# Kernel optimization log

Measured on AMD Instinct MI355X. Metric: run time of the kernel, lower is better.

The kernel has to match this reference:

```python
import jax, jax.numpy as jnp
import numpy as np
import math

# Static configuration (matches init_kwargs / input_specs)
L1 = 2          # lmax of x
L2 = 2          # lmax of y
LZ = L1 + L2    # output lmax = 4
RB = 20         # res_beta (Gauss-Legendre nodes)
RA = 19         # res_alpha (uniform azimuthal samples)
MUL = 128       # input multiplicity per l
C = 128         # num_channels
N = 1024        # batch (nodes/edges)


def _assoc_legendre(l, m, x):
    """Associated Legendre P_l^m(x) with Condon-Shortley phase, via recurrence."""
    pmm = np.ones_like(x)
    if m > 0:
        dfact = float(np.prod(np.arange(1, 2 * m, 2)))  # (2m-1)!!
        pmm = ((-1.0) ** m) * dfact * (1.0 - x * x) ** (m / 2.0)
    if l == m:
        return pmm
    pmmp1 = x * (2 * m + 1) * pmm
    if l == m + 1:
        return pmmp1
    for ll in range(m + 2, l + 1):
        p = ((2 * ll - 1) * x * pmmp1 - (ll + m - 1) * pmm) / (ll - m)
        pmm, pmmp1 = pmmp1, p
    return pmmp1


def _sh_table(L, rb, ra):
    """Orthonormal real spherical harmonics sampled on the (beta, alpha) grid.

    Returns Y [(L+1)^2, rb, ra] and Gauss-Legendre weights qw [rb] such that
    sum_{b,a} f(b,a) Y_lm(b,a) qw[b] * (2*pi/ra) == c_lm exactly for
    bandlimited f (the inverse of the synthesis c -> grid).
    """
    ct, qw = np.polynomial.legendre.leggauss(rb)  # nodes = cos(beta)
    alpha = 2.0 * np.pi * np.arange(ra) / ra
    Y = np.zeros(((L + 1) ** 2, rb, ra))
    for l in range(L + 1):
        for m in range(-l, l + 1):
            am = abs(m)
            nlm = math.sqrt((2 * l + 1) / (4 * math.pi)
                            * math.factorial(l - am) / math.factorial(l + am))
            P = _assoc_legendre(l, am, ct)  # [rb]
            if m == 0:
                ang = np.ones(ra)
            elif m > 0:
                ang = math.sqrt(2.0) * np.cos(m * alpha)
            else:
                ang = math.sqrt(2.0) * np.sin(am * alpha)
            Y[l * l + l + m] = nlm * P[:, None] * ang[None, :]
    return Y, qw


_Y_np, _QW_np = _sh_table(LZ, RB, RA)
Y_TAB = jnp.asarray(_Y_np, jnp.float32)   # [(LZ+1)^2, RB, RA]
QW = jnp.asarray(_QW_np, jnp.float32)     # [RB]


def _per_l_linear_in(v, w, L):
    """Equivariant per-l linear: v [N, mul, (L+1)^2], w [L+1, mul, C] -> [N, C, (L+1)^2]."""
    scale = 1.0 / math.sqrt(v.shape[1])
    outs = [jnp.einsum('nmd,mc->ncd', v[..., l * l:(l + 1) ** 2], w[l]) * scale
            for l in range(L + 1)]
    return jnp.concatenate(outs, axis=-1)


def setup_inputs() -> dict:
    key = jax.random.key(0)
    k0, k1, k2, k3, k4 = jax.random.split(key, 5)
    return {
        'x': jax.random.normal(k0, (N, MUL, (L1 + 1) ** 2), jnp.float32),
        'y': jax.random.normal(k1, (N, MUL, (L2 + 1) ** 2), jnp.float32),
        'wx': jax.random.normal(k2, (L1 + 1, MUL, C), jnp.float32),
        'wy': jax.random.normal(k3, (L2 + 1, MUL, C), jnp.float32),
        'wz': jax.random.normal(k4, (LZ + 1, C, C), jnp.float32),
    }


def reference(x, y, wx, wy, wz):
    # linear_in + mul_to_axis: [N, mul, D] -> [N, C, D]
    xc = _per_l_linear_in(x, wx, L1)  # [N, C, 9]
    yc = _per_l_linear_in(y, wy, L2)  # [N, C, 9]

    # to_s2grid (synthesis): coeffs -> signal on (beta, alpha) grid
    gx = jnp.einsum('ncd,dba->ncba', xc, Y_TAB[:(L1 + 1) ** 2])  # [N,C,RB,RA]
    gy = jnp.einsum('ncd,dba->ncba', yc, Y_TAB[:(L2 + 1) ** 2])

    # pointwise Gaunt product on the grid
    prod = gx * gy

    # from_s2grid (analysis): quadrature projection onto Y_lm up to LZ
    z = jnp.einsum('ncba,dba,b->ncd', prod, Y_TAB, QW) * (2.0 * jnp.pi / RA)  # [N,C,25]

    # axis_to_mul + linear_out_z: per-l channel mixing [C -> C]
    scale = 1.0 / math.sqrt(C)
    outs = [jnp.einsum('ncd,ce->ned', z[..., l * l:(l + 1) ** 2], wz[l]) * scale
            for l in range(LZ + 1)]
    return jnp.concatenate(outs, axis=-1)  # [N, C, 25]
```

## Files before the change

kernel.cpp:

```cpp
#include <hip/hip_runtime.h>
#include <cmath>

#define RB 20
#define RA 19
#define NPT (RB*RA)
#define DZ 25
#define DIN 9
#define MULT 128
#define CH 128

__host__ __device__ constexpr int L_of(int d) { return d == 0 ? 0 : d < 4 ? 1 : d < 9 ? 2 : d < 16 ? 3 : 4; }
__host__ __device__ constexpr int M_of(int d) { return d - L_of(d) * L_of(d) - L_of(d); }
__host__ __device__ constexpr bool gz_nz(int d1, int d2, int dz) {
    const int l1 = L_of(d1), l2 = L_of(d2), l3 = L_of(dz);
    const int m1 = M_of(d1), m2 = M_of(d2), m3 = M_of(dz);
    const int lo = l1 > l2 ? l1 - l2 : l2 - l1;
    if (l3 < lo || l3 > l1 + l2) return false;
    if ((l1 + l2 + l3) & 1) return false;
    const int a1 = m1 < 0 ? -m1 : m1, a2 = m2 < 0 ? -m2 : m2, a3 = m3 < 0 ? -m3 : m3;
    const int sum = a1 + a2, dif = a1 > a2 ? a1 - a2 : a2 - a1;
    if (a3 != sum && a3 != dif) return false;
    if (((m1 < 0) + (m2 < 0) + (m3 < 0)) & 1) return false;
    return true;
}
template<int DZ0, int DZ1>
__host__ __device__ constexpr bool pair_any_r(int d1, int d2) {
    for (int dz = DZ0; dz < DZ1; ++dz) if (gz_nz(d1, d2, dz)) return true;
    return false;
}

static void host_build_gaunt(float* out ) {
    const double PI = 3.14159265358979323846;
    double xq[RB], wq[RB];
    for (int i = 0; i < RB; ++i) {
        double x = cos(PI * (i + 0.75) / (RB + 0.5));
        double dp = 0.0;
        for (int it = 0; it < 100; ++it) {
            double p0 = 1.0, p1 = x;
            for (int k = 2; k <= RB; ++k) {
                double p2 = ((2.0*k - 1.0)*x*p1 - (k - 1.0)*p0) / (double)k;
                p0 = p1; p1 = p2;
            }
            dp = RB * (x*p1 - p0) / (x*x - 1.0);
            double dx = p1 / dp;
            x -= dx;
            if (fabs(dx) < 1e-15) break;
        }
        {
            double p0 = 1.0, p1 = x;
            for (int k = 2; k <= RB; ++k) {
                double p2 = ((2.0*k - 1.0)*x*p1 - (k - 1.0)*p0) / (double)k;
                p0 = p1; p1 = p2;
            }
            dp = RB * (x*p1 - p0) / (x*x - 1.0);
        }
        xq[i] = x;
        wq[i] = 2.0 / ((1.0 - x*x)*dp*dp);
    }
    static double Y[DZ][NPT];
    static double qws[NPT];
    for (int b = 0; b < RB; ++b) {
        double ct = xq[b], st = sqrt(fmax(0.0, 1.0 - ct*ct));
        double P[5][5]; double pmm = 1.0;
        for (int m = 0; m <= 4; ++m) {
            if (m > 0) pmm *= -(2.0*m - 1.0) * st;
            P[m][m] = pmm;
            if (m < 4) {
                double pp = pmm, pc = ct*(2.0*m + 1.0)*pmm;
                P[m+1][m] = pc;
                for (int l = m + 2; l <= 4; ++l) {
                    double pn = ((2.0*l - 1.0)*ct*pc - (double)(l + m - 1)*pp) / (double)(l - m);
                    P[l][m] = pn; pp = pc; pc = pn;
                }
            }
        }
        for (int a = 0; a < RA; ++a) {
            int pt = b*RA + a;
            qws[pt] = wq[b] * (2.0*PI/(double)RA);
            double alpha = 2.0*PI*(double)a/(double)RA;
            for (int l = 0; l <= 4; ++l)
                for (int m = -l; m <= l; ++m) {
                    int am = m < 0 ? -m : m;
                    double fr = 1.0;
                    for (int i = l - am + 1; i <= l + am; ++i) fr *= (double)i;
                    double nlm = sqrt((2.0*l + 1.0) / (4.0*PI) / fr);
                    double ang = (m == 0) ? 1.0
                               : (m > 0 ? sqrt(2.0)*cos(am*alpha) : sqrt(2.0)*sin(am*alpha));
                    Y[l*l + l + m][pt] = nlm * P[l][am] * ang;
                }
        }
    }
    for (int pr = 0; pr < 81; ++pr) {
        int d1 = pr / 9, d2 = pr % 9;
        for (int d = 0; d < DZ; ++d) {
            double s = 0.0;
            for (int p = 0; p < NPT; ++p)
                s += Y[d][p] * Y[d1][p] * Y[d2][p] * qws[p];
            out[pr*28 + d] = gz_nz(d1, d2, d) ? (float)s : 0.0f;
        }
    }
}

template<int DZ0, int DZ1, int D1, int D2, int DZi>
__device__ __forceinline__ void c_dz(const float* __restrict__ g, float p0, float p1,
                                     float* a0, float* a1) {
    if constexpr (DZi < DZ1) {
        if constexpr (gz_nz(D1, D2, DZi)) {
            const float gv = g[(D1 * 9 + D2) * 28 + DZi];
            a0[DZi - DZ0] = fmaf(p0, gv, a0[DZi - DZ0]);
            a1[DZi - DZ0] = fmaf(p1, gv, a1[DZi - DZ0]);
        }
        c_dz<DZ0, DZ1, D1, D2, DZi + 1>(g, p0, p1, a0, a1);
    }
}
template<int DZ0, int DZ1, int D1, int D2>
__device__ __forceinline__ void c_d2(const float* __restrict__ g,
                                     const float* x0, const float* x1,
                                     const float* y0, const float* y1,
                                     float* a0, float* a1) {
    if constexpr (D2 < 9) {
        if constexpr (pair_any_r<DZ0, DZ1>(D1, D2))
            c_dz<DZ0, DZ1, D1, D2, DZ0>(g, x0[D1] * y0[D2], x1[D1] * y1[D2], a0, a1);
        c_d2<DZ0, DZ1, D1, D2 + 1>(g, x0, x1, y0, y1, a0, a1);
    }
}
template<int DZ0, int DZ1, int D1>
__device__ __forceinline__ void c_d1(const float* __restrict__ g,
                                     const float* x0, const float* x1,
                                     const float* y0, const float* y1,
                                     float* a0, float* a1) {
    if constexpr (D1 < 9) {
        c_d2<DZ0, DZ1, D1, 0>(g, x0, x1, y0, y1, a0, a1);
        c_d1<DZ0, DZ1, D1 + 1>(g, x0, x1, y0, y1, a0, a1);
    }
}

template<int D0, int ND, int L0, int NL>
__device__ __forceinline__ void d_tile(const float* sZ, const float* __restrict__ wz,
                                       float* __restrict__ po, int lane) {
    const float s128 = 0.08838834764831845f;
    const int e2 = lane << 1;
    float acc[ND * 4];
    #pragma unroll
    for (int i = 0; i < ND * 4; ++i) acc[i] = 0.f;
    float2 wA[NL * 4], wB[NL * 4];

    #define LOADW_D(W, C0) { \
        _Pragma("unroll") \
        for (int j = 0; j < NL; ++j) { \
            _Pragma("unroll") \
            for (int k = 0; k < 4; ++k) \
                W[j * 4 + k] = *(const float2*)(wz + (L0 + j) * 16384 + ((C0) + k) * 128 + e2); \
        } }
    #define FMA_D(W, C0) { \
        _Pragma("unroll") \
        for (int i = 0; i < ND; ++i) { \
            const int d = D0 + i; \
            const int l = (d == 0) ? 0 : (d < 4) ? 1 : (d < 9) ? 2 : (d < 16) ? 3 : 4; \
            float4 z0 = *(const float4*)(sZ + d * 128 + (C0));           \
            float4 z1 = *(const float4*)(sZ + (25 + d) * 128 + (C0));    \
            _Pragma("unroll") \
            for (int k = 0; k < 4; ++k) { \
                float zc0 = (k == 0) ? z0.x : (k == 1) ? z0.y : (k == 2) ? z0.z : z0.w; \
                float zc1 = (k == 0) ? z1.x : (k == 1) ? z1.y : (k == 2) ? z1.z : z1.w; \
                acc[i*4+0] = fmaf(zc0, W[(l - L0) * 4 + k].x, acc[i*4+0]); \
                acc[i*4+1] = fmaf(zc0, W[(l - L0) * 4 + k].y, acc[i*4+1]); \
                acc[i*4+2] = fmaf(zc1, W[(l - L0) * 4 + k].x, acc[i*4+2]); \
                acc[i*4+3] = fmaf(zc1, W[(l - L0) * 4 + k].y, acc[i*4+3]); \
            } \
        } }

    LOADW_D(wA, 0);
    for (int c0 = 0; c0 < CH; c0 += 8) {
        LOADW_D(wB, c0 + 4);
        FMA_D(wA, c0);
        if (c0 < CH - 8) LOADW_D(wA, c0 + 8);
        FMA_D(wB, c0 + 4);
    }
    #undef LOADW_D
    #undef FMA_D

    #pragma unroll
    for (int i = 0; i < ND; ++i) {
        po[e2 * 25 + D0 + i]              = acc[i*4+0] * s128;
        po[(e2 + 1) * 25 + D0 + i]        = acc[i*4+1] * s128;
        po[3200 + e2 * 25 + D0 + i]       = acc[i*4+2] * s128;
        po[3200 + (e2 + 1) * 25 + D0 + i] = acc[i*4+3] * s128;
    }
}

__global__ __launch_bounds__(256) void gaunt_fused(
    const float* __restrict__ xg, const float* __restrict__ yg,
    const float* __restrict__ wxg, const float* __restrict__ wyg,
    const float* __restrict__ wzg, float* __restrict__ outg,
    const float* __restrict__ gGt) {

    __shared__ __align__(16) float pool[17884];
    float* sZ  = pool;
    float* sXY = pool + 6400;
    float* sXc = pool + 11008;
    float* sG  = pool + 15616;

    const int tid  = threadIdx.x;
    const int b    = blockIdx.x;
    const int lane = tid & 63;
    const int wave = __builtin_amdgcn_readfirstlane(tid >> 6);
    const float s128 = 0.08838834764831845f;

    {
        const float4* xs = (const float4*)(xg + 2 * b * 1152);
        const float4* ys = (const float4*)(yg + 2 * b * 1152);
        for (int i = tid; i < 1152; i += 256) {
            float4 v = (i < 576) ? xs[i] : ys[i - 576];
            int r = (i < 576) ? i : i - 576;
            int base = (i < 576) ? 0 : 2304;
            int j0 = r * 4;
            #pragma unroll
            for (int k = 0; k < 4; ++k) {
                int j = j0 + k;
                int n = j / 1152;
                int jj = j - n * 1152;
                int m = jj / 9, d = jj - 9 * m;
                float val = (k == 0) ? v.x : (k == 1) ? v.y : (k == 2) ? v.z : v.w;
                sXY[base + n * 1152 + d * 128 + m] = val;
            }
        }
        for (int i = tid; i < 567; i += 256)
            ((float4*)sG)[i] = ((const float4*)gGt)[i];
    }
    __syncthreads();

    {
        const int side = wave >> 1, n = wave & 1;
        const int c2 = lane << 1;
        const float* wb = side ? wyg : wxg;
        const float* xb = sXY + side * 2304 + n * 1152;
        float acc[18];
        #pragma unroll
        for (int i = 0; i < 18; ++i) acc[i] = 0.f;
        float2 wA[12], wB[12];

        #define LOADW_B(W, M0) { \
            _Pragma("unroll") \
            for (int k = 0; k < 4; ++k) { \
                W[k]     = *(const float2*)(wb + ((M0) + k) * 128 + c2); \
                W[4 + k] = *(const float2*)(wb + 16384 + ((M0) + k) * 128 + c2); \
                W[8 + k] = *(const float2*)(wb + 32768 + ((M0) + k) * 128 + c2); \
            } }
        #define FMA_B(W, M0) { \
            _Pragma("unroll") \
            for (int d = 0; d < 9; ++d) { \
                const int lb = (d == 0) ? 0 : (d < 4) ? 4 : 8; \
                float4 xv = *(const float4*)(xb + d * 128 + (M0));    \
                acc[d*2+0] = fmaf(xv.x, W[lb+0].x, acc[d*2+0]); \
                acc[d*2+0] = fmaf(xv.y, W[lb+1].x, acc[d*2+0]); \
                acc[d*2+0] = fmaf(xv.z, W[lb+2].x, acc[d*2+0]); \
                acc[d*2+0] = fmaf(xv.w, W[lb+3].x, acc[d*2+0]); \
                acc[d*2+1] = fmaf(xv.x, W[lb+0].y, acc[d*2+1]); \
                acc[d*2+1] = fmaf(xv.y, W[lb+1].y, acc[d*2+1]); \
                acc[d*2+1] = fmaf(xv.z, W[lb+2].y, acc[d*2+1]); \
                acc[d*2+1] = fmaf(xv.w, W[lb+3].y, acc[d*2+1]); \
            } }

        LOADW_B(wA, 0);
        for (int m0 = 0; m0 < MULT; m0 += 8) {
            LOADW_B(wB, m0 + 4);
            FMA_B(wA, m0);
            if (m0 < MULT - 8) LOADW_B(wA, m0 + 8);
            FMA_B(wB, m0 + 4);
        }
        #undef LOADW_B
        #undef FMA_B

        #pragma unroll
        for (int d = 0; d < 9; ++d) {
            float2 v = make_float2(acc[d*2+0] * s128, acc[d*2+1] * s128);
            *(float2*)(sXc + ((side * 9 + d) * 2 + n) * 128 + c2) = v;
        }
    }
    __syncthreads();

    {
        const int c = tid & 127;
        const int half = __builtin_amdgcn_readfirstlane(tid >> 7);
        float xr0[9], xr1[9], yr0[9], yr1[9];
        #pragma unroll
        for (int d = 0; d < 9; ++d) {
            xr0[d] = sXc[(d * 2 + 0) * 128 + c];
            xr1[d] = sXc[(d * 2 + 1) * 128 + c];
            yr0[d] = sXc[((9 + d) * 2 + 0) * 128 + c];
            yr1[d] = sXc[((9 + d) * 2 + 1) * 128 + c];
        }
        if (half == 0) {
            float a0[12], a1[12];
            #pragma unroll
            for (int i = 0; i < 12; ++i) { a0[i] = 0.f; a1[i] = 0.f; }
            c_d1<0, 12, 0>(sG, xr0, xr1, yr0, yr1, a0, a1);
            #pragma unroll
            for (int i = 0; i < 12; ++i) {
                sZ[i * 128 + c]        = a0[i];
                sZ[(25 + i) * 128 + c] = a1[i];
            }
        } else {
            float a0[13], a1[13];
            #pragma unroll
            for (int i = 0; i < 13; ++i) { a0[i] = 0.f; a1[i] = 0.f; }
            c_d1<12, 25, 0>(sG, xr0, xr1, yr0, yr1, a0, a1);
            #pragma unroll
            for (int i = 0; i < 13; ++i) {
                sZ[(12 + i) * 128 + c] = a0[i];
                sZ[(37 + i) * 128 + c] = a1[i];
            }
        }
    }
    __syncthreads();

    float* po = outg + 2 * b * (CH * DZ);
    if      (wave == 0) d_tile<0,  4, 0, 2>(sZ, wzg, po, lane);
    else if (wave == 1) d_tile<4,  5, 2, 1>(sZ, wzg, po, lane);
    else if (wave == 2) d_tile<9,  7, 3, 1>(sZ, wzg, po, lane);
    else                d_tile<16, 9, 4, 1>(sZ, wzg, po, lane);
}

extern "C" void kernel_launch(void* const* d_in, const int* in_sizes, int n_in,
                              void* d_out, int out_size, void* d_ws, size_t ws_size,
                              hipStream_t stream) {
    static float h_gGt[81 * 28];
    static bool built = false;
    if (!built) { host_build_gaunt(h_gGt); built = true; }
    hipMemcpyAsync(d_ws, h_gGt, sizeof(h_gGt), hipMemcpyHostToDevice, stream);

    int N = in_sizes[0] / (MULT * DIN);

    hipLaunchKernelGGL(gaunt_fused, dim3(N / 2), dim3(256), 0, stream,
                       (const float*)d_in[0], (const float*)d_in[1],
                       (const float*)d_in[2], (const float*)d_in[3],
                       (const float*)d_in[4], (float*)d_out, (const float*)d_ws);
}
```

Baseline: 115.4 us.

## Process four nodes per block to amortize weight loads across more rows

Each block now handles four batch rows instead of two. Every weight element loaded from global memory in the input-linear and output-linear stages is reused across four nodes, which halves weight traffic per node. The cost is larger shared memory (about 134KB), more accumulators per thread, and a launch bound of one block per CU. The grid also shrinks to 256 blocks, which lowers occupancy and latency hiding on a GPU with many CUs.

```diff
diff --git a/kernel.cpp b/kernel.cpp
--- a/kernel.cpp
+++ b/kernel.cpp
@@ -136,13 +136,13 @@
 }
 
 template<int D0, int ND, int L0, int NL>
-__device__ __forceinline__ void d_tile(const float* sZ, const float* __restrict__ wz,
-                                       float* __restrict__ po, int lane) {
+__device__ __forceinline__ void d_tile4(const float* sZ, const float* __restrict__ wz,
+                                        float* __restrict__ outp, int lane) {
     const float s128 = 0.08838834764831845f;
     const int e2 = lane << 1;
-    float acc[ND * 4];
+    float acc[ND * 8];
     #pragma unroll
-    for (int i = 0; i < ND * 4; ++i) acc[i] = 0.f;
+    for (int i = 0; i < ND * 8; ++i) acc[i] = 0.f;
     float2 wA[NL * 4], wB[NL * 4];
 
     #define LOADW_D(W, C0) { \
@@ -157,63 +157,63 @@
         for (int i = 0; i < ND; ++i) { \
             const int d = D0 + i; \
             const int l = (d == 0) ? 0 : (d < 4) ? 1 : (d < 9) ? 2 : (d < 16) ? 3 : 4; \
-            float4 z0 = *(const float4*)(sZ + d * 128 + (C0));           \
-            float4 z1 = *(const float4*)(sZ + (25 + d) * 128 + (C0));    \
             _Pragma("unroll") \
-            for (int k = 0; k < 4; ++k) { \
-                float zc0 = (k == 0) ? z0.x : (k == 1) ? z0.y : (k == 2) ? z0.z : z0.w; \
-                float zc1 = (k == 0) ? z1.x : (k == 1) ? z1.y : (k == 2) ? z1.z : z1.w; \
-                acc[i*4+0] = fmaf(zc0, W[(l - L0) * 4 + k].x, acc[i*4+0]); \
-                acc[i*4+1] = fmaf(zc0, W[(l - L0) * 4 + k].y, acc[i*4+1]); \
-                acc[i*4+2] = fmaf(zc1, W[(l - L0) * 4 + k].x, acc[i*4+2]); \
-                acc[i*4+3] = fmaf(zc1, W[(l - L0) * 4 + k].y, acc[i*4+3]); \
+            for (int n = 0; n < 4; ++n) { \
+                float4 z4 = *(const float4*)(sZ + (n * 25 + d) * 128 + (C0));   \
+                _Pragma("unroll") \
+                for (int k = 0; k < 4; ++k) { \
+                    float zc = (k == 0) ? z4.x : (k == 1) ? z4.y : (k == 2) ? z4.z : z4.w; \
+                    acc[(i*4+n)*2+0] = fmaf(zc, W[(l - L0) * 4 + k].x, acc[(i*4+n)*2+0]); \
+                    acc[(i*4+n)*2+1] = fmaf(zc, W[(l - L0) * 4 + k].y, acc[(i*4+n)*2+1]); \
+                } \
             } \
         } }
 
     LOADW_D(wA, 0);
+    LOADW_D(wB, 4);
     for (int c0 = 0; c0 < CH; c0 += 8) {
-        LOADW_D(wB, c0 + 4);
         FMA_D(wA, c0);
-        if (c0 < CH - 8) LOADW_D(wA, c0 + 8);
+        if (c0 + 8 < CH) LOADW_D(wA, c0 + 8);
         FMA_D(wB, c0 + 4);
+        if (c0 + 12 < CH) LOADW_D(wB, c0 + 12);
     }
     #undef LOADW_D
     #undef FMA_D
 
     #pragma unroll
-    for (int i = 0; i < ND; ++i) {
-        po[e2 * 25 + D0 + i]              = acc[i*4+0] * s128;
-        po[(e2 + 1) * 25 + D0 + i]        = acc[i*4+1] * s128;
-        po[3200 + e2 * 25 + D0 + i]       = acc[i*4+2] * s128;
-        po[3200 + (e2 + 1) * 25 + D0 + i] = acc[i*4+3] * s128;
-    }
-}
-
-__global__ __launch_bounds__(256) void gaunt_fused(
+    for (int i = 0; i < ND; ++i)
+        #pragma unroll
+        for (int n = 0; n < 4; ++n) {
+            outp[n * 3200 + e2 * 25 + D0 + i]       = acc[(i*4+n)*2+0] * s128;
+            outp[n * 3200 + (e2 + 1) * 25 + D0 + i] = acc[(i*4+n)*2+1] * s128;
+        }
+}
+
+__global__ __launch_bounds__(256, 1) void gaunt_fused(
     const float* __restrict__ xg, const float* __restrict__ yg,
     const float* __restrict__ wxg, const float* __restrict__ wyg,
     const float* __restrict__ wzg, float* __restrict__ outg,
     const float* __restrict__ gGt) {
 
-    __shared__ __align__(16) float pool[17884];
-    float* sZ  = pool;
-    float* sXY = pool + 6400;
-    float* sXc = pool + 11008;
-    float* sG  = pool + 15616;
+    __shared__ __align__(16) float pool[33500];
+    float* sXY = pool;
+    float* sXc = pool + 9216;
+    float* sZ  = pool + 18432;
+    float* sG  = pool + 31232;
 
     const int tid  = threadIdx.x;
-    const int b    = blockIdx.x;
+    const int nb4  = blockIdx.x * 4;
     const int lane = tid & 63;
     const int wave = __builtin_amdgcn_readfirstlane(tid >> 6);
     const float s128 = 0.08838834764831845f;
 
     {
-        const float4* xs = (const float4*)(xg + 2 * b * 1152);
-        const float4* ys = (const float4*)(yg + 2 * b * 1152);
-        for (int i = tid; i < 1152; i += 256) {
-            float4 v = (i < 576) ? xs[i] : ys[i - 576];
-            int r = (i < 576) ? i : i - 576;
-            int base = (i < 576) ? 0 : 2304;
+        const float4* xs = (const float4*)(xg + (size_t)nb4 * 1152);
+        const float4* ys = (const float4*)(yg + (size_t)nb4 * 1152);
+        for (int i = tid; i < 2304; i += 256) {
+            float4 v = (i < 1152) ? xs[i] : ys[i - 1152];
+            int r = (i < 1152) ? i : i - 1152;
+            int base = (i < 1152) ? 0 : 4608;
             int j0 = r * 4;
             #pragma unroll
             for (int k = 0; k < 4; ++k) {
@@ -231,95 +231,98 @@
     __syncthreads();
 
     {
-        const int side = wave >> 1, n = wave & 1;
-        const int c2 = lane << 1;
+        const int side = wave >> 1, ch = wave & 1;
+        const int c = ch * 64 + lane;
         const float* wb = side ? wyg : wxg;
-        const float* xb = sXY + side * 2304 + n * 1152;
-        float acc[18];
+        const float* xb = sXY + side * 4608;
+        float acc[36];
         #pragma unroll
-        for (int i = 0; i < 18; ++i) acc[i] = 0.f;
-        float2 wA[12], wB[12];
+        for (int i = 0; i < 36; ++i) acc[i] = 0.f;
+        float wA[12], wB[12];
 
         #define LOADW_B(W, M0) { \
             _Pragma("unroll") \
             for (int k = 0; k < 4; ++k) { \
-                W[k]     = *(const float2*)(wb + ((M0) + k) * 128 + c2); \
-                W[4 + k] = *(const float2*)(wb + 16384 + ((M0) + k) * 128 + c2); \
-                W[8 + k] = *(const float2*)(wb + 32768 + ((M0) + k) * 128 + c2); \
+                W[k]     = wb[((M0) + k) * 128 + c]; \
+                W[4 + k] = wb[16384 + ((M0) + k) * 128 + c]; \
+                W[8 + k] = wb[32768 + ((M0) + k) * 128 + c]; \
             } }
         #define FMA_B(W, M0) { \
             _Pragma("unroll") \
             for (int d = 0; d < 9; ++d) { \
                 const int lb = (d == 0) ? 0 : (d < 4) ? 4 : 8; \
-                float4 xv = *(const float4*)(xb + d * 128 + (M0));    \
-                acc[d*2+0] = fmaf(xv.x, W[lb+0].x, acc[d*2+0]); \
-                acc[d*2+0] = fmaf(xv.y, W[lb+1].x, acc[d*2+0]); \
-                acc[d*2+0] = fmaf(xv.z, W[lb+2].x, acc[d*2+0]); \
-                acc[d*2+0] = fmaf(xv.w, W[lb+3].x, acc[d*2+0]); \
-                acc[d*2+1] = fmaf(xv.x, W[lb+0].y, acc[d*2+1]); \
-                acc[d*2+1] = fmaf(xv.y, W[lb+1].y, acc[d*2+1]); \
-                acc[d*2+1] = fmaf(xv.z, W[lb+2].y, acc[d*2+1]); \
-                acc[d*2+1] = fmaf(xv.w, W[lb+3].y, acc[d*2+1]); \
+                _Pragma("unroll") \
+                for (int n = 0; n < 4; ++n) { \
+                    float4 xv = *(const float4*)(xb + n * 1152 + d * 128 + (M0));   \
+                    acc[d*4+n] = fmaf(xv.x, W[lb+0], acc[d*4+n]); \
+                    acc[d*4+n] = fmaf(xv.y, W[lb+1], acc[d*4+n]); \
+                    acc[d*4+n] = fmaf(xv.z, W[lb+2], acc[d*4+n]); \
+                    acc[d*4+n] = fmaf(xv.w, W[lb+3], acc[d*4+n]); \
+                } \
             } }
 
         LOADW_B(wA, 0);
+        LOADW_B(wB, 4);
         for (int m0 = 0; m0 < MULT; m0 += 8) {
-            LOADW_B(wB, m0 + 4);
             FMA_B(wA, m0);
-            if (m0 < MULT - 8) LOADW_B(wA, m0 + 8);
+            if (m0 + 8 < MULT) LOADW_B(wA, m0 + 8);
             FMA_B(wB, m0 + 4);
+            if (m0 + 12 < MULT) LOADW_B(wB, m0 + 12);
         }
         #undef LOADW_B
         #undef FMA_B
 
         #pragma unroll
-        for (int d = 0; d < 9; ++d) {
-            float2 v = make_float2(acc[d*2+0] * s128, acc[d*2+1] * s128);
-            *(float2*)(sXc + ((side * 9 + d) * 2 + n) * 128 + c2) = v;
-        }
+        for (int d = 0; d < 9; ++d)
+            #pragma unroll
+            for (int n = 0; n < 4; ++n)
+                sXc[((side * 9 + d) * 4 + n) * 128 + c] = acc[d*4+n] * s128;
     }
     __syncthreads();
 
     {
         const int c = tid & 127;
         const int half = __builtin_amdgcn_readfirstlane(tid >> 7);
-        float xr0[9], xr1[9], yr0[9], yr1[9];
         #pragma unroll
-        for (int d = 0; d < 9; ++d) {
-            xr0[d] = sXc[(d * 2 + 0) * 128 + c];
-            xr1[d] = sXc[(d * 2 + 1) * 128 + c];
-            yr0[d] = sXc[((9 + d) * 2 + 0) * 128 + c];
-            yr1[d] = sXc[((9 + d) * 2 + 1) * 128 + c];
-        }
-        if (half == 0) {
-            float a0[12], a1[12];
+        for (int np = 0; np < 2; ++np) {
+            float xr0[9], xr1[9], yr0[9], yr1[9];
             #pragma unroll
-            for (int i = 0; i < 12; ++i) { a0[i] = 0.f; a1[i] = 0.f; }
-            c_d1<0, 12, 0>(sG, xr0, xr1, yr0, yr1, a0, a1);
-            #pragma unroll
-            for (int i = 0; i < 12; ++i) {
-                sZ[i * 128 + c]        = a0[i];
-                sZ[(25 + i) * 128 + c] = a1[i];
-            }
-        } else {
-            float a0[13], a1[13];
-            #pragma unroll
-            for (int i = 0; i < 13; ++i) { a0[i] = 0.f; a1[i] = 0.f; }
-            c_d1<12, 25, 0>(sG, xr0, xr1, yr0, yr1, a0, a1);
-            #pragma unroll
-            for (int i = 0; i < 13; ++i) {
-                sZ[(12 + i) * 128 + c] = a0[i];
-                sZ[(37 + i) * 128 + c] = a1[i];
+            for (int d = 0; d < 9; ++d) {
+                xr0[d] = sXc[(d * 4 + np * 2 + 0) * 128 + c];
+                xr1[d] = sXc[(d * 4 + np * 2 + 1) * 128 + c];
+                yr0[d] = sXc[((9 + d) * 4 + np * 2 + 0) * 128 + c];
+                yr1[d] = sXc[((9 + d) * 4 + np * 2 + 1) * 128 + c];
+            }
+            if (half == 0) {
+                float a0[12], a1[12];
+                #pragma unroll
+                for (int i = 0; i < 12; ++i) { a0[i] = 0.f; a1[i] = 0.f; }
+                c_d1<0, 12, 0>(sG, xr0, xr1, yr0, yr1, a0, a1);
+                #pragma unroll
+                for (int i = 0; i < 12; ++i) {
+                    sZ[((np * 2 + 0) * 25 + i) * 128 + c] = a0[i];
+                    sZ[((np * 2 + 1) * 25 + i) * 128 + c] = a1[i];
+                }
+            } else {
+                float a0[13], a1[13];
+                #pragma unroll
+                for (int i = 0; i < 13; ++i) { a0[i] = 0.f; a1[i] = 0.f; }
+                c_d1<12, 25, 0>(sG, xr0, xr1, yr0, yr1, a0, a1);
+                #pragma unroll
+                for (int i = 0; i < 13; ++i) {
+                    sZ[((np * 2 + 0) * 25 + 12 + i) * 128 + c] = a0[i];
+                    sZ[((np * 2 + 1) * 25 + 12 + i) * 128 + c] = a1[i];
+                }
             }
         }
     }
     __syncthreads();
 
-    float* po = outg + 2 * b * (CH * DZ);
-    if      (wave == 0) d_tile<0,  4, 0, 2>(sZ, wzg, po, lane);
-    else if (wave == 1) d_tile<4,  5, 2, 1>(sZ, wzg, po, lane);
-    else if (wave == 2) d_tile<9,  7, 3, 1>(sZ, wzg, po, lane);
-    else                d_tile<16, 9, 4, 1>(sZ, wzg, po, lane);
+    float* po = outg + (size_t)nb4 * (CH * DZ);
+    if      (wave == 0) d_tile4<0,  4, 0, 2>(sZ, wzg, po, lane);
+    else if (wave == 1) d_tile4<4,  5, 2, 1>(sZ, wzg, po, lane);
+    else if (wave == 2) d_tile4<9,  7, 3, 1>(sZ, wzg, po, lane);
+    else                d_tile4<16, 9, 4, 1>(sZ, wzg, po, lane);
 }
 
 extern "C" void kernel_launch(void* const* d_in, const int* in_sizes, int n_in,
@@ -332,7 +335,7 @@
 
     int N = in_sizes[0] / (MULT * DIN);
 
-    hipLaunchKernelGGL(gaunt_fused, dim3(N / 2), dim3(256), 0, stream,
+    hipLaunchKernelGGL(gaunt_fused, dim3(N / 4), dim3(256), 0, stream,
                        (const float*)d_in[0], (const float*)d_in[1],
                        (const float*)d_in[2], (const float*)d_in[3],
                        (const float*)d_in[4], (float*)d_out, (const float*)d_ws);
```

After: 122.8 us. 1.06x slower.

## Drop LDS transpose, remap linear-in to channel-per-lane, deepen weight prefetch

Applied to the files above, without the earlier changes.

The input staging now copies x and y into shared memory in their native [n][m][d] order instead of transposing into d-major layout. The linear-in stage is remapped so each lane owns one channel for both nodes, reading the inputs via broadcast float4 LDS loads. Weight loads in both matmul stages change from float2 per lane to two scalar loads, with four register buffers for a deeper prefetch. Launch bounds now request 2 blocks per SM, which may force register spilling given the larger register arrays.

```diff
diff --git a/kernel.cpp b/kernel.cpp
--- a/kernel.cpp
+++ b/kernel.cpp
@@ -139,18 +139,19 @@
 __device__ __forceinline__ void d_tile(const float* sZ, const float* __restrict__ wz,
                                        float* __restrict__ po, int lane) {
     const float s128 = 0.08838834764831845f;
-    const int e2 = lane << 1;
     float acc[ND * 4];
     #pragma unroll
     for (int i = 0; i < ND * 4; ++i) acc[i] = 0.f;
-    float2 wA[NL * 4], wB[NL * 4];
+    float W0[NL * 8], W1[NL * 8], W2[NL * 8], W3[NL * 8];
 
     #define LOADW_D(W, C0) { \
         _Pragma("unroll") \
         for (int j = 0; j < NL; ++j) { \
             _Pragma("unroll") \
-            for (int k = 0; k < 4; ++k) \
-                W[j * 4 + k] = *(const float2*)(wz + (L0 + j) * 16384 + ((C0) + k) * 128 + e2); \
+            for (int k = 0; k < 4; ++k) { \
+                W[j*8 + k*2 + 0] = wz[(L0 + j) * 16384 + ((C0) + k) * 128 + lane]; \
+                W[j*8 + k*2 + 1] = wz[(L0 + j) * 16384 + ((C0) + k) * 128 + lane + 64]; \
+            } \
         } }
     #define FMA_D(W, C0) { \
         _Pragma("unroll") \
@@ -161,35 +162,37 @@
             float4 z1 = *(const float4*)(sZ + (25 + d) * 128 + (C0));    \
             _Pragma("unroll") \
             for (int k = 0; k < 4; ++k) { \
+                float wa = W[(l - L0)*8 + k*2 + 0]; \
+                float wb = W[(l - L0)*8 + k*2 + 1]; \
                 float zc0 = (k == 0) ? z0.x : (k == 1) ? z0.y : (k == 2) ? z0.z : z0.w; \
                 float zc1 = (k == 0) ? z1.x : (k == 1) ? z1.y : (k == 2) ? z1.z : z1.w; \
-                acc[i*4+0] = fmaf(zc0, W[(l - L0) * 4 + k].x, acc[i*4+0]); \
-                acc[i*4+1] = fmaf(zc0, W[(l - L0) * 4 + k].y, acc[i*4+1]); \
-                acc[i*4+2] = fmaf(zc1, W[(l - L0) * 4 + k].x, acc[i*4+2]); \
-                acc[i*4+3] = fmaf(zc1, W[(l - L0) * 4 + k].y, acc[i*4+3]); \
+                acc[i*4+0] = fmaf(zc0, wa, acc[i*4+0]); \
+                acc[i*4+1] = fmaf(zc0, wb, acc[i*4+1]); \
+                acc[i*4+2] = fmaf(zc1, wa, acc[i*4+2]); \
+                acc[i*4+3] = fmaf(zc1, wb, acc[i*4+3]); \
             } \
         } }
 
-    LOADW_D(wA, 0);
-    for (int c0 = 0; c0 < CH; c0 += 8) {
-        LOADW_D(wB, c0 + 4);
-        FMA_D(wA, c0);
-        if (c0 < CH - 8) LOADW_D(wA, c0 + 8);
-        FMA_D(wB, c0 + 4);
+    LOADW_D(W0, 0); LOADW_D(W1, 4); LOADW_D(W2, 8); LOADW_D(W3, 12);
+    for (int c0 = 0; c0 < CH; c0 += 16) {
+        FMA_D(W0, c0);        if (c0 + 16 < CH) LOADW_D(W0, c0 + 16);
+        FMA_D(W1, c0 + 4);    if (c0 + 20 < CH) LOADW_D(W1, c0 + 20);
+        FMA_D(W2, c0 + 8);    if (c0 + 24 < CH) LOADW_D(W2, c0 + 24);
+        FMA_D(W3, c0 + 12);   if (c0 + 28 < CH) LOADW_D(W3, c0 + 28);
     }
     #undef LOADW_D
     #undef FMA_D
 
     #pragma unroll
     for (int i = 0; i < ND; ++i) {
-        po[e2 * 25 + D0 + i]              = acc[i*4+0] * s128;
-        po[(e2 + 1) * 25 + D0 + i]        = acc[i*4+1] * s128;
-        po[3200 + e2 * 25 + D0 + i]       = acc[i*4+2] * s128;
-        po[3200 + (e2 + 1) * 25 + D0 + i] = acc[i*4+3] * s128;
-    }
-}
-
-__global__ __launch_bounds__(256) void gaunt_fused(
+        po[lane * 25 + D0 + i]               = acc[i*4+0] * s128;
+        po[(lane + 64) * 25 + D0 + i]        = acc[i*4+1] * s128;
+        po[3200 + lane * 25 + D0 + i]        = acc[i*4+2] * s128;
+        po[3200 + (lane + 64) * 25 + D0 + i] = acc[i*4+3] * s128;
+    }
+}
+
+__global__ __launch_bounds__(256, 2) void gaunt_fused(
     const float* __restrict__ xg, const float* __restrict__ yg,
     const float* __restrict__ wxg, const float* __restrict__ wyg,
     const float* __restrict__ wzg, float* __restrict__ outg,
@@ -208,22 +211,13 @@
     const float s128 = 0.08838834764831845f;
 
     {
-        const float4* xs = (const float4*)(xg + 2 * b * 1152);
-        const float4* ys = (const float4*)(yg + 2 * b * 1152);
-        for (int i = tid; i < 1152; i += 256) {
-            float4 v = (i < 576) ? xs[i] : ys[i - 576];
-            int r = (i < 576) ? i : i - 576;
-            int base = (i < 576) ? 0 : 2304;
-            int j0 = r * 4;
-            #pragma unroll
-            for (int k = 0; k < 4; ++k) {
-                int j = j0 + k;
-                int n = j / 1152;
-                int jj = j - n * 1152;
-                int m = jj / 9, d = jj - 9 * m;
-                float val = (k == 0) ? v.x : (k == 1) ? v.y : (k == 2) ? v.z : v.w;
-                sXY[base + n * 1152 + d * 128 + m] = val;
-            }
+        const float4* xs4 = (const float4*)(xg + (size_t)(2 * b) * 1152);
+        const float4* ys4 = (const float4*)(yg + (size_t)(2 * b) * 1152);
+        float4* dst = (float4*)sXY;
+        #pragma unroll
+        for (int t = 0; t < 5; ++t) {
+            int i = tid + t * 256;
+            if (i < 1152) dst[i] = (i < 576) ? xs4[i] : ys4[i - 576];
         }
         for (int i = tid; i < 567; i += 256)
             ((float4*)sG)[i] = ((const float4*)gGt)[i];
@@ -231,51 +225,57 @@
     __syncthreads();
 
     {
-        const int side = wave >> 1, n = wave & 1;
-        const int c2 = lane << 1;
+        const int side = wave >> 1, ch = wave & 1;
+        const int c = ch * 64 + lane;
         const float* wb = side ? wyg : wxg;
-        const float* xb = sXY + side * 2304 + n * 1152;
+        const float* xL0 = sXY + side * 2304;
+        const float* xL1 = sXY + side * 2304 + 1152;
         float acc[18];
         #pragma unroll
         for (int i = 0; i < 18; ++i) acc[i] = 0.f;
-        float2 wA[12], wB[12];
+        float W0[12], W1[12], W2[12], W3[12];
 
         #define LOADW_B(W, M0) { \
             _Pragma("unroll") \
             for (int k = 0; k < 4; ++k) { \
-                W[k]     = *(const float2*)(wb + ((M0) + k) * 128 + c2); \
-                W[4 + k] = *(const float2*)(wb + 16384 + ((M0) + k) * 128 + c2); \
-                W[8 + k] = *(const float2*)(wb + 32768 + ((M0) + k) * 128 + c2); \
+                W[k]     = wb[((M0) + k) * 128 + c]; \
+                W[4 + k] = wb[16384 + ((M0) + k) * 128 + c]; \
+                W[8 + k] = wb[32768 + ((M0) + k) * 128 + c]; \
             } }
         #define FMA_B(W, M0) { \
+            float xs0[36], xs1[36]; \
+            _Pragma("unroll") \
+            for (int j = 0; j < 9; ++j) { \
+                *(float4*)(xs0 + j * 4) = *(const float4*)(xL0 + (M0) * 9 + j * 4); \
+                *(float4*)(xs1 + j * 4) = *(const float4*)(xL1 + (M0) * 9 + j * 4); \
+            } \
             _Pragma("unroll") \
             for (int d = 0; d < 9; ++d) { \
                 const int lb = (d == 0) ? 0 : (d < 4) ? 4 : 8; \
-                float4 xv = *(const float4*)(xb + d * 128 + (M0));    \
-                acc[d*2+0] = fmaf(xv.x, W[lb+0].x, acc[d*2+0]); \
-                acc[d*2+0] = fmaf(xv.y, W[lb+1].x, acc[d*2+0]); \
-                acc[d*2+0] = fmaf(xv.z, W[lb+2].x, acc[d*2+0]); \
-                acc[d*2+0] = fmaf(xv.w, W[lb+3].x, acc[d*2+0]); \
-                acc[d*2+1] = fmaf(xv.x, W[lb+0].y, acc[d*2+1]); \
-                acc[d*2+1] = fmaf(xv.y, W[lb+1].y, acc[d*2+1]); \
-                acc[d*2+1] = fmaf(xv.z, W[lb+2].y, acc[d*2+1]); \
-                acc[d*2+1] = fmaf(xv.w, W[lb+3].y, acc[d*2+1]); \
+                acc[d*2+0] = fmaf(xs0[0*9+d], W[lb+0], acc[d*2+0]); \
+                acc[d*2+0] = fmaf(xs0[1*9+d], W[lb+1], acc[d*2+0]); \
+                acc[d*2+0] = fmaf(xs0[2*9+d], W[lb+2], acc[d*2+0]); \
+                acc[d*2+0] = fmaf(xs0[3*9+d], W[lb+3], acc[d*2+0]); \
+                acc[d*2+1] = fmaf(xs1[0*9+d], W[lb+0], acc[d*2+1]); \
+                acc[d*2+1] = fmaf(xs1[1*9+d], W[lb+1], acc[d*2+1]); \
+                acc[d*2+1] = fmaf(xs1[2*9+d], W[lb+2], acc[d*2+1]); \
+                acc[d*2+1] = fmaf(xs1[3*9+d], W[lb+3], acc[d*2+1]); \
             } }
 
-        LOADW_B(wA, 0);
-        for (int m0 = 0; m0 < MULT; m0 += 8) {
-            LOADW_B(wB, m0 + 4);
-            FMA_B(wA, m0);
-            if (m0 < MULT - 8) LOADW_B(wA, m0 + 8);
-            FMA_B(wB, m0 + 4);
+        LOADW_B(W0, 0); LOADW_B(W1, 4); LOADW_B(W2, 8); LOADW_B(W3, 12);
+        for (int m0 = 0; m0 < MULT; m0 += 16) {
+            FMA_B(W0, m0);        if (m0 + 16 < MULT) LOADW_B(W0, m0 + 16);
+            FMA_B(W1, m0 + 4);    if (m0 + 20 < MULT) LOADW_B(W1, m0 + 20);
+            FMA_B(W2, m0 + 8);    if (m0 + 24 < MULT) LOADW_B(W2, m0 + 24);
+            FMA_B(W3, m0 + 12);   if (m0 + 28 < MULT) LOADW_B(W3, m0 + 28);
         }
         #undef LOADW_B
         #undef FMA_B
 
         #pragma unroll
         for (int d = 0; d < 9; ++d) {
-            float2 v = make_float2(acc[d*2+0] * s128, acc[d*2+1] * s128);
-            *(float2*)(sXc + ((side * 9 + d) * 2 + n) * 128 + c2) = v;
+            sXc[((side * 9 + d) * 2 + 0) * 128 + c] = acc[d*2+0] * s128;
+            sXc[((side * 9 + d) * 2 + 1) * 128 + c] = acc[d*2+1] * s128;
         }
     }
     __syncthreads();
```

Result: slower. 408.8 us (+254.2%).
